# Kernel tuning notes

Measured on AMD Instinct MI355X. Metric: run time of the kernel, lower is better.

The kernel has to match this reference:

```python
import jax, jax.numpy as jnp
import numpy as np

EPS = 1e-6
NEG = 1e9

def _norm(x):
    # Normalizator math with alpha=1, gamma=0 (torch.std is unbiased -> ddof=1)
    m = jnp.mean(x, axis=-1, keepdims=True)
    s = jnp.std(x, axis=-1, ddof=1, keepdims=True)
    return (x - m) / (s + EPS)

def setup_inputs() -> dict:
    key = jax.random.key(0)
    ks = jax.random.split(key, 16)
    T, S, D, F, L = 4096, 4096, 512, 2048, 4
    sc = 1.0 / np.sqrt(D)
    scf = 1.0 / np.sqrt(F)
    return {
        "current_tgt_output": jax.random.normal(ks[0], (T, D), jnp.float32),
        "encoder_output": jax.random.normal(ks[1], (S, D), jnp.float32),
        "cross_mask": jax.random.randint(ks[2], (T, S), 0, 2).astype(jnp.float32),
        "Wq": jax.random.normal(ks[3], (L, D, D), jnp.float32) * sc,
        "Wk": jax.random.normal(ks[4], (L, D, D), jnp.float32) * sc,
        "Wv": jax.random.normal(ks[5], (L, D, D), jnp.float32) * sc,
        "Wo": jax.random.normal(ks[6], (L, D, D), jnp.float32) * sc,
        "Cq": jax.random.normal(ks[7], (L, D, D), jnp.float32) * sc,
        "Ck": jax.random.normal(ks[8], (L, D, D), jnp.float32) * sc,
        "Cv": jax.random.normal(ks[9], (L, D, D), jnp.float32) * sc,
        "Co": jax.random.normal(ks[10], (L, D, D), jnp.float32) * sc,
        "W1": jax.random.normal(ks[11], (L, D, F), jnp.float32) * sc,
        "W2": jax.random.normal(ks[12], (L, F, D), jnp.float32) * scf,
        "alpha": jnp.ones((1,), jnp.float32),
        "gamma": jnp.zeros((1,), jnp.float32),
        "input_ids": jax.random.randint(ks[13], (T,), 0, S),
        "training_step": T,
        "training_mode": 1,
    }

def reference(current_tgt_output, encoder_output, cross_mask, Wq, Wk, Wv, Wo,
              Cq, Ck, Cv, Co, W1, W2, alpha, gamma, input_ids,
              training_step, training_mode):
    T = training_step
    x = current_tgt_output[:T] if training_mode else current_tgt_output
    cm = cross_mask[:T]                                  # [T, S]
    # the python double-loop -> single vectorized gather: self_mask[i,k]=cross_mask[i, input_ids[k]]
    self_mask = cm[:, input_ids]                         # [T, T]
    sbias = (self_mask - 1.0) * NEG                      # additive mask bias
    cbias = (cm - 1.0) * NEG
    D = x.shape[-1]
    scale = 1.0 / jnp.sqrt(jnp.asarray(D, x.dtype))
    L = Wq.shape[0]
    for l in range(L):
        h = _norm(x)
        q, k, v = h @ Wq[l], h @ Wk[l], h @ Wv[l]
        a = jax.nn.softmax(q @ k.T * scale + sbias, axis=-1)
        x = x + (a @ v) @ Wo[l]
        h = _norm(x)
        q = h @ Cq[l]
        k, v = encoder_output @ Ck[l], encoder_output @ Cv[l]
        a = jax.nn.softmax(q @ k.T * scale + cbias, axis=-1)
        x = x + (a @ v) @ Co[l]
        h = _norm(x)
        x = x + jax.nn.relu(h @ W1[l]) @ W2[l]
    return alpha * _norm(x) + gamma
```

## Files before the change

kernel.cpp:

```cpp
#include <hip/hip_runtime.h>
#include <math.h>

typedef _Float16 half_t;
typedef unsigned int u32;
typedef unsigned short u16;
typedef float f32x4 __attribute__((ext_vector_type(4)));
typedef _Float16 f16x8 __attribute__((ext_vector_type(8)));
typedef _Float16 f16x4 __attribute__((ext_vector_type(4)));

#define T_DIM 4096
#define S_DIM 4096
#define D_DIM 512
#define F_DIM 2048
#define NLAYER 4
#define KVS ((size_t)4096 * 512)

__device__ __forceinline__ void gload16(const void* g, void* l) {
    __builtin_amdgcn_global_load_lds(
        (const __attribute__((address_space(1))) u32*)g,
        (__attribute__((address_space(3))) u32*)l, 16, 0, 0);
}

template<int N> __device__ __forceinline__ void wait_vm() {
    if constexpr (N == 0) asm volatile("s_waitcnt vmcnt(0)" ::: "memory");
    else if constexpr (N == 3) asm volatile("s_waitcnt vmcnt(3)" ::: "memory");
    else if constexpr (N == 4) asm volatile("s_waitcnt vmcnt(4)" ::: "memory");
    else if constexpr (N == 6) asm volatile("s_waitcnt vmcnt(6)" ::: "memory");
    else if constexpr (N == 8) asm volatile("s_waitcnt vmcnt(8)" ::: "memory");
}

template<int BN, int EPI>
__global__ __launch_bounds__(512)
void gemm_nt(const half_t* __restrict__ A, int lda,
             const half_t* __restrict__ B, int ldb,
             int N, int K, int gx,
             const float* __restrict__ Cin, float* __restrict__ Cout,
             half_t* __restrict__ D1, half_t* __restrict__ D2,
             half_t* __restrict__ D3, int ldd)
{
    constexpr int BM = 128, BK = 64;
    constexpr int NF = BN / 32;
    constexpr int LPT = 2 + BN / 64;
    constexpr int NSLOT = (BN == 64) ? 3 : 2;
    __shared__ half_t As[NSLOT][BM * BK];
    __shared__ half_t Bs[NSLOT][BN * BK];

    const int tid  = threadIdx.x;
    const int wave = tid >> 6;
    const int lane = tid & 63;

    const int nb  = gridDim.x;
    const int bid = blockIdx.x;
    const int nid = (bid & 7) * (nb >> 3) + (bid >> 3);
    const int gy  = nb / gx;
    const int bx  = nid % gx;
    const int by  = nid / gx % gy;
    const int bm = by * BM, bn = bx * BN;

    const int wm = (wave >> 1) * 32;
    const int wn = (wave & 1) * (BN / 2);
    const int kq = lane >> 4;
    const int rr = lane & 15;
    const int scol = (((lane & 7) ^ (lane >> 3)) << 3);

    f32x4 acc[2][NF];
#pragma unroll
    for (int m = 0; m < 2; ++m)
#pragma unroll
        for (int n = 0; n < NF; ++n)
            acc[m][n] = f32x4{0.f, 0.f, 0.f, 0.f};

    auto stage = [&](int buf, int k0) {
#pragma unroll
        for (int c = 0; c < 2; ++c) {
            const int row = wave * 16 + c * 8 + (lane >> 3);
            gload16(A + (size_t)(bm + row) * lda + k0 + scol,
                    (char*)&As[buf][0] + (wave * 2 + c) * 1024 + lane * 16);
        }
        if constexpr (BN == 64) {
            const int row = wave * 8 + (lane >> 3);
            gload16(B + (size_t)(bn + row) * ldb + k0 + scol,
                    (char*)&Bs[buf][0] + wave * 1024 + lane * 16);
        } else {
#pragma unroll
            for (int c = 0; c < 2; ++c) {
                const int row = wave * 16 + c * 8 + (lane >> 3);
                gload16(B + (size_t)(bn + row) * ldb + k0 + scol,
                        (char*)&Bs[buf][0] + (wave * 2 + c) * 1024 + lane * 16);
            }
        }
    };

    const int nt = K / BK;
    stage(0, 0);
    if constexpr (NSLOT == 3) stage(1, BK);
    int cur = 0, pf = NSLOT - 1;
    for (int t = 0; t < nt; ++t) {
        if (t + 1 < nt) wait_vm<(NSLOT - 2) * LPT>(); else wait_vm<0>();
        __builtin_amdgcn_s_barrier();
        if (t + NSLOT - 1 < nt) stage(pf, (t + NSLOT - 1) * BK);
#pragma unroll
        for (int ks = 0; ks < 2; ++ks) {
            f16x8 af[2], bf[NF];
#pragma unroll
            for (int m = 0; m < 2; ++m) {
                const int r = wm + m * 16 + rr;
                af[m] = *(const f16x8*)&As[cur][r * BK + (((ks * 4 + kq) ^ (r & 7)) << 3)];
            }
#pragma unroll
            for (int n = 0; n < NF; ++n) {
                const int r = wn + n * 16 + rr;
                bf[n] = *(const f16x8*)&Bs[cur][r * BK + (((ks * 4 + kq) ^ (r & 7)) << 3)];
            }
#pragma unroll
            for (int m = 0; m < 2; ++m)
#pragma unroll
                for (int n = 0; n < NF; ++n)
                    acc[m][n] = __builtin_amdgcn_mfma_f32_16x16x32_f16(af[m], bf[n], acc[m][n], 0, 0, 0);
        }
        cur = (cur + 1 == NSLOT) ? 0 : cur + 1;
        pf  = (pf  + 1 == NSLOT) ? 0 : pf  + 1;
    }

    const int r0 = bm + wm + (lane >> 4) * 4;
#pragma unroll
    for (int m = 0; m < 2; ++m)
#pragma unroll
        for (int n = 0; n < NF; ++n) {
            const int c = bn + wn + n * 16 + rr;
            if (EPI == 1) {
#pragma unroll
                for (int i = 0; i < 4; ++i) {
                    const int r = r0 + m * 16 + i;
                    Cout[(size_t)r * N + c] = Cin[(size_t)r * N + c] + acc[m][n][i];
                }
            } else if (EPI == 2) {
#pragma unroll
                for (int i = 0; i < 4; ++i)
                    D1[(size_t)(r0 + m * 16 + i) * ldd + c] = (half_t)acc[m][n][i];
            } else if (EPI == 5) {
                if (bn < 512) {
#pragma unroll
                    for (int i = 0; i < 4; ++i)
                        D1[(size_t)(r0 + m * 16 + i) * 512 + c] = (half_t)acc[m][n][i];
                } else if (bn < 1024) {
#pragma unroll
                    for (int i = 0; i < 4; ++i)
                        D2[(size_t)(r0 + m * 16 + i) * 512 + (c - 512)] = (half_t)acc[m][n][i];
                } else {
                    f16x4 hv;
#pragma unroll
                    for (int i = 0; i < 4; ++i) hv[i] = (half_t)acc[m][n][i];
                    *(f16x4*)&D3[(size_t)(c - 1024) * ldd + r0 + m * 16] = hv;
                }
            } else {
                const int l = c >> 10;
                const int sub = c & 1023;
                if (sub < 512) {
#pragma unroll
                    for (int i = 0; i < 4; ++i)
                        D2[l * KVS + (size_t)(r0 + m * 16 + i) * 512 + sub] = (half_t)acc[m][n][i];
                } else {
                    f16x4 hv;
#pragma unroll
                    for (int i = 0; i < 4; ++i) hv[i] = (half_t)acc[m][n][i];
                    *(f16x4*)&D3[l * KVS + (size_t)(sub - 512) * 4096 + r0 + m * 16] = hv;
                }
            }
        }
}

template<int EPI, int SPLITK = 1, int P16 = 1>
__global__ __launch_bounds__(256)
void gemm97(const half_t* __restrict__ A, int lda,
            const half_t* __restrict__ B, int ldb,
            int K, int gx, half_t* __restrict__ D,
            float* __restrict__ Fout, int ldd)
{
    constexpr int BK = 32, NSLOT = 3, LPT = 4;
    __shared__ half_t As[NSLOT][128 * BK];
    __shared__ half_t Bs[NSLOT][128 * BK];

    const int tid  = threadIdx.x;
    const int wave = tid >> 6;
    const int lane = tid & 63;

    const int nb  = gridDim.x;
    const int bid = blockIdx.x;
    const int nid = (bid & 7) * (nb >> 3) + (bid >> 3);
    const int gy  = nb / (gx * SPLITK);
    const int bx  = nid % gx;
    const int tmp = nid / gx;
    const int by  = tmp % gy;
    const int kz  = tmp / gy;
    const int bm = by * 128, bn = bx * 128;

    const int Keff = K / SPLITK;
    A += (size_t)kz * Keff;
    B += (size_t)kz * Keff;

    const int wm = (wave >> 1) * 64;
    const int wn = (wave & 1) * 64;
    const int kq = lane >> 4;
    const int rr = lane & 15;
    const int srow = lane >> 2;
    const int scol = (((lane & 3) ^ ((lane >> 3) & 3)) << 3);
    const int kqa  = kq ^ ((rr >> 1) & 3);

    const half_t* Abase = A + (size_t)(bm + wave * 16 + srow) * lda + scol;
    const half_t* Bbase = B + (size_t)(bn + wave * 16 + srow) * ldb + scol;

    f32x4 acc[4][4];
#pragma unroll
    for (int m = 0; m < 4; ++m)
#pragma unroll
        for (int n = 0; n < 4; ++n)
            acc[m][n] = f32x4{0.f, 0.f, 0.f, 0.f};

    auto stage = [&](int buf, int k0) {
#pragma unroll
        for (int c = 0; c < 2; ++c)
            gload16(Abase + (size_t)c * 64 * lda + k0,
                    (char*)&As[buf][0] + c * 4096 + wave * 1024 + lane * 16);
#pragma unroll
        for (int c = 0; c < 2; ++c)
            gload16(Bbase + (size_t)c * 64 * ldb + k0,
                    (char*)&Bs[buf][0] + c * 4096 + wave * 1024 + lane * 16);
    };

    const int nt = Keff / BK;
    stage(0, 0);
    stage(1, BK);
    int cur = 0, pf = 2;
    for (int t = 0; t < nt; ++t) {
        if (t + 1 < nt) wait_vm<LPT>(); else wait_vm<0>();
        __builtin_amdgcn_s_barrier();
        if (t + 2 < nt) stage(pf, (t + 2) * BK);
        f16x8 af[4], bf[4];
#pragma unroll
        for (int m = 0; m < 4; ++m)
            af[m] = *(const f16x8*)&As[cur][(wm + m * 16 + rr) * BK + kqa * 8];
#pragma unroll
        for (int n = 0; n < 4; ++n)
            bf[n] = *(const f16x8*)&Bs[cur][(wn + n * 16 + rr) * BK + kqa * 8];
#pragma unroll
        for (int m = 0; m < 4; ++m)
#pragma unroll
            for (int n = 0; n < 4; ++n)
                acc[m][n] = __builtin_amdgcn_mfma_f32_16x16x32_f16(af[m], bf[n], acc[m][n], 0, 0, 0);
        cur = (cur == 2) ? 0 : cur + 1;
        pf  = (pf  == 2) ? 0 : pf + 1;
    }

    const int r0 = bm + wm + (lane >> 4) * 4;
    const int soff = kz * gx * 128;
#pragma unroll
    for (int m = 0; m < 4; ++m)
#pragma unroll
        for (int n = 0; n < 4; ++n) {
            const int c = bn + wn + n * 16 + rr;
#pragma unroll
            for (int i = 0; i < 4; ++i) {
                float v = acc[m][n][i];
                const size_t r = r0 + m * 16 + i;
                if constexpr (SPLITK > 1) {
                    if constexpr (P16) D[r * ldd + soff + c] = (half_t)v;
                    else               Fout[r * ldd + soff + c] = v;
                } else {
                    if (EPI == 4) v = fmaxf(v, 0.f);
                    D[r * ldd + c] = (half_t)v;
                }
            }
        }
}

__global__ __launch_bounds__(256)
void reduce_p16(const half_t* __restrict__ P, half_t* __restrict__ ao)
{
    const size_t q = ((size_t)blockIdx.x * 256 + threadIdx.x) * 8;
    const size_t r = q >> 9;
    const int d = (int)(q & 511);
    const half_t* row = P + r * 2048 + d;
    float s[8] = {0.f};
#pragma unroll
    for (int j = 0; j < 4; ++j) {
        f16x8 v = *(const f16x8*)(row + j * 512);
#pragma unroll
        for (int e = 0; e < 8; ++e) s[e] += (float)v[e];
    }
    f16x8 o;
#pragma unroll
    for (int e = 0; e < 8; ++e) o[e] = (half_t)s[e];
    *(f16x8*)&ao[q] = o;
}

template<int FINAL>
__global__ __launch_bounds__(256)
void norm_red(const float* __restrict__ xin, const float* __restrict__ P,
              float* __restrict__ xbuf, half_t* __restrict__ hh,
              float* __restrict__ outF, const float* __restrict__ alphaP,
              const float* __restrict__ gammaP)
{
    const int row  = blockIdx.x * 4 + (threadIdx.x >> 6);
    const int lane = threadIdx.x & 63;
    const int d0 = lane * 8;
    const float* xr = xin + (size_t)row * D_DIM + d0;
    float v[8];
    {
        float4 a = *(const float4*)xr;
        float4 b = *(const float4*)(xr + 4);
        v[0]=a.x; v[1]=a.y; v[2]=a.z; v[3]=a.w; v[4]=b.x; v[5]=b.y; v[6]=b.z; v[7]=b.w;
    }
    const float* pr = P + (size_t)row * 2048 + d0;
#pragma unroll
    for (int j = 0; j < 4; ++j) {
        float4 a = *(const float4*)(pr + j * 512);
        float4 b = *(const float4*)(pr + j * 512 + 4);
        v[0]+=a.x; v[1]+=a.y; v[2]+=a.z; v[3]+=a.w; v[4]+=b.x; v[5]+=b.y; v[6]+=b.z; v[7]+=b.w;
    }
    float* xo = xbuf + (size_t)row * D_DIM + d0;
    *(float4*)xo       = float4{v[0], v[1], v[2], v[3]};
    *(float4*)(xo + 4) = float4{v[4], v[5], v[6], v[7]};

    float s = 0.f;
#pragma unroll
    for (int j = 0; j < 8; ++j) s += v[j];
#pragma unroll
    for (int off = 32; off; off >>= 1) s += __shfl_xor(s, off);
    const float mean = s * (1.f / 512.f);
    float ss = 0.f;
#pragma unroll
    for (int j = 0; j < 8; ++j) { float d = v[j] - mean; ss += d * d; }
#pragma unroll
    for (int off = 32; off; off >>= 1) ss += __shfl_xor(ss, off);
    const float inv = 1.f / (sqrtf(ss * (1.f / 511.f)) + 1e-6f);
    if (FINAL) {
        const float alp = alphaP[0], gam = gammaP[0];
        float o[8];
#pragma unroll
        for (int j = 0; j < 8; ++j) o[j] = alp * ((v[j] - mean) * inv) + gam;
        float* op = outF + (size_t)row * D_DIM + d0;
        *(float4*)op       = float4{o[0], o[1], o[2], o[3]};
        *(float4*)(op + 4) = float4{o[4], o[5], o[6], o[7]};
    } else {
        f16x8 hv;
#pragma unroll
        for (int j = 0; j < 8; ++j) hv[j] = (half_t)((v[j] - mean) * inv);
        *(f16x8*)&hh[(size_t)row * D_DIM + d0] = hv;
    }
}

template<int FINAL>
__global__ __launch_bounds__(256)
void norm_rows(const float* __restrict__ x, half_t* __restrict__ hh,
               float* __restrict__ outF, const float* __restrict__ alphaP,
               const float* __restrict__ gammaP)
{
    const int row  = blockIdx.x * 4 + (threadIdx.x >> 6);
    const int lane = threadIdx.x & 63;
    const float* xr = x + (size_t)row * D_DIM + lane * 8;
    float4 a = *(const float4*)xr;
    float4 b = *(const float4*)(xr + 4);
    float v[8] = {a.x, a.y, a.z, a.w, b.x, b.y, b.z, b.w};
    float s = 0.f;
#pragma unroll
    for (int j = 0; j < 8; ++j) s += v[j];
#pragma unroll
    for (int off = 32; off; off >>= 1) s += __shfl_xor(s, off);
    const float mean = s * (1.f / 512.f);
    float ss = 0.f;
#pragma unroll
    for (int j = 0; j < 8; ++j) { float d = v[j] - mean; ss += d * d; }
#pragma unroll
    for (int off = 32; off; off >>= 1) ss += __shfl_xor(ss, off);
    const float inv = 1.f / (sqrtf(ss * (1.f / 511.f)) + 1e-6f);
    if (FINAL) {
        const float alp = alphaP[0], gam = gammaP[0];
        float o[8];
#pragma unroll
        for (int j = 0; j < 8; ++j) o[j] = alp * ((v[j] - mean) * inv) + gam;
        float* op = outF + (size_t)row * D_DIM + lane * 8;
        *(float4*)op       = float4{o[0], o[1], o[2], o[3]};
        *(float4*)(op + 4) = float4{o[4], o[5], o[6], o[7]};
    } else {
        f16x8 hv;
#pragma unroll
        for (int j = 0; j < 8; ++j) hv[j] = (half_t)((v[j] - mean) * inv);
        *(f16x8*)&hh[(size_t)row * D_DIM + lane * 8] = hv;
    }
}

__global__ __launch_bounds__(256)
void cast_f16(const float* __restrict__ in, half_t* __restrict__ out)
{
    size_t i = ((size_t)blockIdx.x * 256 + threadIdx.x) * 8;
    float4 a = *(const float4*)&in[i];
    float4 b = *(const float4*)&in[i + 4];
    float v[8] = {a.x, a.y, a.z, a.w, b.x, b.y, b.z, b.w};
    f16x8 o;
#pragma unroll
    for (int j = 0; j < 8; ++j) o[j] = (half_t)v[j];
    *(f16x8*)&out[i] = o;
}

__global__ __launch_bounds__(256)
void transpose_cast(const float* __restrict__ in, half_t* __restrict__ out,
                    int R, int C, float scale, int inZ, int outZ)
{
    in  += (size_t)blockIdx.z * inZ;
    out += (size_t)blockIdx.z * outZ;
    __shared__ float tile[32][33];
    const int tx = threadIdx.x & 31, ty = threadIdx.x >> 5;
    const int r0 = blockIdx.y * 32, c0 = blockIdx.x * 32;
#pragma unroll
    for (int i = 0; i < 4; ++i)
        tile[ty + i * 8][tx] = in[(size_t)(r0 + ty + i * 8) * C + c0 + tx];
    __syncthreads();
#pragma unroll
    for (int i = 0; i < 4; ++i)
        out[(size_t)(c0 + ty + i * 8) * R + r0 + tx] = (half_t)(tile[tx][ty + i * 8] * scale);
}

__global__ __launch_bounds__(256)
void pack_masks(const float* __restrict__ cm, const int* __restrict__ ids,
                u32* __restrict__ crossb, u32* __restrict__ selfb)
{
    const int t = blockIdx.x;
    const float* row = cm + (size_t)t * S_DIM;
    __shared__ u32 cb[S_DIM / 32];
    __shared__ u16 sh16[256];
    const int tid = threadIdx.x;
    u32 bits = 0;
#pragma unroll
    for (int q = 0; q < 4; ++q) {
        float4 v = *(const float4*)&row[tid * 16 + q * 4];
        bits |= (v.x > 0.5f ? 1u : 0u) << (q * 4 + 0);
        bits |= (v.y > 0.5f ? 1u : 0u) << (q * 4 + 1);
        bits |= (v.z > 0.5f ? 1u : 0u) << (q * 4 + 2);
        bits |= (v.w > 0.5f ? 1u : 0u) << (q * 4 + 3);
    }
    ((u16*)cb)[tid] = (u16)bits;
    __syncthreads();
    u32 sb = 0;
#pragma unroll
    for (int q = 0; q < 4; ++q) {
        int4 id4 = *(const int4*)&ids[tid * 16 + q * 4];
        sb |= ((cb[id4.x >> 5] >> (id4.x & 31)) & 1u) << (q * 4 + 0);
        sb |= ((cb[id4.y >> 5] >> (id4.y & 31)) & 1u) << (q * 4 + 1);
        sb |= ((cb[id4.z >> 5] >> (id4.z & 31)) & 1u) << (q * 4 + 2);
        sb |= ((cb[id4.w >> 5] >> (id4.w & 31)) & 1u) << (q * 4 + 3);
    }
    sh16[tid] = (u16)sb;
    __syncthreads();
    if (tid < 128) {
        crossb[(size_t)t * 128 + tid] = cb[tid];
        selfb[(size_t)t * 128 + tid]  = (u32)sh16[2 * tid] | ((u32)sh16[2 * tid + 1] << 16);
    }
}

__global__ __launch_bounds__(256)
void softmax_rows16(half_t* __restrict__ logits, const u32* __restrict__ bits)
{
    const int t = blockIdx.x;
    half_t* row = logits + (size_t)t * S_DIM;
    const u32* bw = bits + (size_t)t * (S_DIM / 32);
    __shared__ float red[8];
    const int tid = threadIdx.x, wave = tid >> 6, lane = tid & 63;
    const int s0 = tid * 16;
    f16x8 h0 = *(const f16x8*)&row[s0];
    f16x8 h1 = *(const f16x8*)&row[s0 + 8];
    const u32 w = bw[tid >> 1] >> ((tid & 1) * 16);
    float z[16];
    float lmax = -3.0e38f;
#pragma unroll
    for (int q = 0; q < 16; ++q) {
        const float v = (float)((q < 8) ? h0[q & 7] : h1[q & 7]);
        z[q] = v + (((w >> q) & 1u) ? 0.f : -1e9f);
        lmax = fmaxf(lmax, z[q]);
    }
#pragma unroll
    for (int off = 32; off; off >>= 1) lmax = fmaxf(lmax, __shfl_xor(lmax, off));
    if (lane == 0) red[wave] = lmax;
    __syncthreads();
    const float mx = fmaxf(fmaxf(red[0], red[1]), fmaxf(red[2], red[3]));
    float lsum = 0.f;
#pragma unroll
    for (int q = 0; q < 16; ++q) { z[q] = __expf(z[q] - mx); lsum += z[q]; }
#pragma unroll
    for (int off = 32; off; off >>= 1) lsum += __shfl_xor(lsum, off);
    if (lane == 0) red[4 + wave] = lsum;
    __syncthreads();
    const float inv = 1.f / (red[4] + red[5] + red[6] + red[7]);
    f16x8 o0, o1;
#pragma unroll
    for (int q = 0; q < 8; ++q) {
        o0[q] = (half_t)(z[q] * inv);
        o1[q] = (half_t)(z[q + 8] * inv);
    }
    *(f16x8*)&row[s0] = o0;
    *(f16x8*)&row[s0 + 8] = o1;
}

extern "C" void kernel_launch(void* const* d_in, const int* in_sizes, int n_in,
                              void* d_out, int out_size, void* d_ws, size_t ws_size,
                              hipStream_t stream)
{
    (void)in_sizes; (void)n_in; (void)out_size; (void)ws_size;

    const float* x0p  = (const float*)d_in[0];
    const float* encp = (const float*)d_in[1];
    const float* cmp  = (const float*)d_in[2];
    const float* Wq = (const float*)d_in[3], *Wk = (const float*)d_in[4];
    const float* Wv = (const float*)d_in[5], *Wo = (const float*)d_in[6];
    const float* Cq = (const float*)d_in[7], *Ck = (const float*)d_in[8];
    const float* Cv = (const float*)d_in[9], *Co = (const float*)d_in[10];
    const float* W1p = (const float*)d_in[11];
    const float* W2p = (const float*)d_in[12];
    const float* alphap = (const float*)d_in[13];
    const float* gammap = (const float*)d_in[14];
    const int*   idsp   = (const int*)d_in[15];
    float* outp = (float*)d_out;

    char* wp = (char*)d_ws;
    auto take = [&](size_t nelem, int esz) -> void* {
        void* p = (void*)wp;
        wp += (nelem * (size_t)esz + 255) & ~(size_t)255;
        return p;
    };
    half_t* wqkvT = (half_t*)take((size_t)NLAYER * 1536 * 512, 2);
    half_t* ckvT  = (half_t*)take((size_t)NLAYER * 1024 * 512, 2);
    half_t* cqT   = (half_t*)take((size_t)NLAYER * 512 * 512, 2);
    half_t* woT   = (half_t*)take((size_t)NLAYER * 512 * 512, 2);
    half_t* coT   = (half_t*)take((size_t)NLAYER * 512 * 512, 2);
    half_t* w1T   = (half_t*)take((size_t)NLAYER * D_DIM * F_DIM, 2);
    half_t* w2T   = (half_t*)take((size_t)NLAYER * D_DIM * F_DIM, 2);
    half_t* hh    = (half_t*)take((size_t)T_DIM * D_DIM, 2);
    half_t* qb    = (half_t*)take((size_t)T_DIM * D_DIM, 2);
    half_t* kb    = (half_t*)take((size_t)S_DIM * D_DIM, 2);
    half_t* vT    = (half_t*)take((size_t)S_DIM * D_DIM, 2);
    half_t* ao    = (half_t*)take((size_t)T_DIM * D_DIM, 2);
    half_t* mid   = (half_t*)take((size_t)T_DIM * F_DIM, 2);
    half_t* enc16 = (half_t*)take((size_t)S_DIM * D_DIM, 2);
    half_t* kbC   = (half_t*)take((size_t)NLAYER * S_DIM * D_DIM, 2);
    half_t* vTC   = (half_t*)take((size_t)NLAYER * S_DIM * D_DIM, 2);
    float* xbuf   = (float*)take((size_t)T_DIM * D_DIM, 4);
    half_t* logit16 = (half_t*)take((size_t)T_DIM * S_DIM, 2);
    half_t* p16   = (half_t*)take((size_t)T_DIM * 2048, 2);
    float* pbuf   = (float*)take((size_t)T_DIM * 2048, 4);
    u32* crossb = (u32*)take((size_t)T_DIM * (S_DIM / 32), 4);
    u32* selfb  = (u32*)take((size_t)T_DIM * (S_DIM / 32), 4);

    const dim3 B(256), B512(512);
    const float qscale = 0.04419417382415922f;

    const int SQ = 512 * 512, QKVZ = 1536 * 512, KVZ = 1024 * 512, FZ = 512 * 2048;
    transpose_cast<<<dim3(16,16,4), B, 0, stream>>>(Wq, wqkvT,            512, 512, qscale, SQ, QKVZ);
    transpose_cast<<<dim3(16,16,4), B, 0, stream>>>(Wk, wqkvT + SQ,       512, 512, 1.f,    SQ, QKVZ);
    transpose_cast<<<dim3(16,16,4), B, 0, stream>>>(Wv, wqkvT + 2 * SQ,   512, 512, 1.f,    SQ, QKVZ);
    transpose_cast<<<dim3(16,16,4), B, 0, stream>>>(Wo, woT,              512, 512, 1.f,    SQ, SQ);
    transpose_cast<<<dim3(16,16,4), B, 0, stream>>>(Cq, cqT,              512, 512, qscale, SQ, SQ);
    transpose_cast<<<dim3(16,16,4), B, 0, stream>>>(Ck, ckvT,             512, 512, 1.f,    SQ, KVZ);
    transpose_cast<<<dim3(16,16,4), B, 0, stream>>>(Cv, ckvT + SQ,        512, 512, 1.f,    SQ, KVZ);
    transpose_cast<<<dim3(16,16,4), B, 0, stream>>>(Co, coT,              512, 512, 1.f,    SQ, SQ);
    transpose_cast<<<dim3(64,16,4), B, 0, stream>>>(W1p, w1T, 512, 2048, 1.f, FZ, FZ);
    transpose_cast<<<dim3(16,64,4), B, 0, stream>>>(W2p, w2T, 2048, 512, 1.f, FZ, FZ);
    cast_f16<<<dim3((S_DIM * D_DIM / 8) / 256), B, 0, stream>>>(encp, enc16);
    pack_masks<<<dim3(T_DIM), B, 0, stream>>>(cmp, idsp, crossb, selfb);
    gemm_nt<64, 7><<<dim3(2048), B512, 0, stream>>>(enc16, 512, ckvT, 512,
        4096, 512, 64, nullptr, nullptr, nullptr, kbC, vTC, 4096);

    for (int l = 0; l < NLAYER; ++l) {
        const float* xin = (l == 0) ? x0p : xbuf;

        if (l == 0)
            norm_rows<0><<<T_DIM / 4, B, 0, stream>>>(x0p, hh, nullptr, nullptr, nullptr);
        else
            norm_red<0><<<T_DIM / 4, B, 0, stream>>>(xbuf, pbuf, xbuf, hh, nullptr, nullptr, nullptr);

        gemm_nt<64, 5><<<dim3(768), B512, 0, stream>>>(hh, 512, wqkvT + (size_t)l * QKVZ, 512,
            1536, 512, 24, nullptr, nullptr, qb, kb, vT, 4096);
        gemm97<2><<<dim3(1024), B, 0, stream>>>(qb, 512, kb, 512, 512, 32, logit16, nullptr, 4096);
        softmax_rows16<<<dim3(T_DIM), B, 0, stream>>>(logit16, selfb);
        gemm97<0, 4, 1><<<dim3(512), B, 0, stream>>>(logit16, 4096, vT, 4096,
            4096, 4, p16, nullptr, 2048);
        reduce_p16<<<dim3(1024), B, 0, stream>>>(p16, ao);
        gemm_nt<64, 1><<<dim3(256), B512, 0, stream>>>(ao, 512, woT + (size_t)l * SQ, 512,
            512, 512, 8, xin, xbuf, nullptr, nullptr, nullptr, 0);

        norm_rows<0><<<T_DIM / 4, B, 0, stream>>>(xbuf, hh, nullptr, nullptr, nullptr);
        gemm_nt<64, 2><<<dim3(256), B512, 0, stream>>>(hh, 512, cqT + (size_t)l * SQ, 512,
            512, 512, 8, nullptr, nullptr, qb, nullptr, nullptr, 512);
        gemm97<2><<<dim3(1024), B, 0, stream>>>(qb, 512, kbC + (size_t)l * KVS, 512,
            512, 32, logit16, nullptr, 4096);
        softmax_rows16<<<dim3(T_DIM), B, 0, stream>>>(logit16, crossb);
        gemm97<0, 4, 1><<<dim3(512), B, 0, stream>>>(logit16, 4096, vTC + (size_t)l * KVS, 4096,
            4096, 4, p16, nullptr, 2048);
        reduce_p16<<<dim3(1024), B, 0, stream>>>(p16, ao);
        gemm_nt<64, 1><<<dim3(256), B512, 0, stream>>>(ao, 512, coT + (size_t)l * SQ, 512,
            512, 512, 8, xbuf, xbuf, nullptr, nullptr, nullptr, 0);

        norm_rows<0><<<T_DIM / 4, B, 0, stream>>>(xbuf, hh, nullptr, nullptr, nullptr);
        gemm97<4><<<dim3(512), B, 0, stream>>>(hh, 512, w1T + (size_t)l * FZ, 512,
            512, 16, mid, nullptr, 2048);
        gemm97<0, 4, 0><<<dim3(512), B, 0, stream>>>(mid, 2048, w2T + (size_t)l * FZ, 2048,
            2048, 4, nullptr, pbuf, 2048);
    }

    norm_red<1><<<T_DIM / 4, B, 0, stream>>>(xbuf, pbuf, xbuf, nullptr, outp, alphap, gammap);
}
```

Before: 1.091 ms.

## Fold output projections into V and fuse residual-add with layer norm

Uses (A·V)·Wo = A·(V·Wo) to precompute V·Wo, and Cv-projected encoder values times Co, with a new gemm_fold kernel that writes transposed values. This removes the per-attention reduce kernel and the output-projection GEMM. The split-K partial sums are now reduced in a fused attn_tail kernel that adds the residual and computes the next layer norm in one pass, replacing reduce_p16, the output projection and norm_rows. In exchange the V·Wo products are rounded to fp16 before the attention GEMM, which may change numerics slightly.

```diff
diff --git a/kernel.cpp b/kernel.cpp
--- a/kernel.cpp
+++ b/kernel.cpp
@@ -34,7 +34,6 @@
 void gemm_nt(const half_t* __restrict__ A, int lda,
              const half_t* __restrict__ B, int ldb,
              int N, int K, int gx,
-             const float* __restrict__ Cin, float* __restrict__ Cout,
              half_t* __restrict__ D1, half_t* __restrict__ D2,
              half_t* __restrict__ D3, int ldd)
 {
@@ -52,9 +51,8 @@
     const int nb  = gridDim.x;
     const int bid = blockIdx.x;
     const int nid = (bid & 7) * (nb >> 3) + (bid >> 3);
-    const int gy  = nb / gx;
     const int bx  = nid % gx;
-    const int by  = nid / gx % gy;
+    const int by  = nid / gx;
     const int bm = by * BM, bn = bx * BN;
 
     const int wm = (wave >> 1) * 32;
@@ -128,45 +126,115 @@
 #pragma unroll
         for (int n = 0; n < NF; ++n) {
             const int c = bn + wn + n * 16 + rr;
-            if (EPI == 1) {
-#pragma unroll
-                for (int i = 0; i < 4; ++i) {
-                    const int r = r0 + m * 16 + i;
-                    Cout[(size_t)r * N + c] = Cin[(size_t)r * N + c] + acc[m][n][i];
-                }
-            } else if (EPI == 2) {
+            if (EPI == 2) {
 #pragma unroll
                 for (int i = 0; i < 4; ++i)
                     D1[(size_t)(r0 + m * 16 + i) * ldd + c] = (half_t)acc[m][n][i];
             } else if (EPI == 5) {
-                if (bn < 512) {
-#pragma unroll
-                    for (int i = 0; i < 4; ++i)
-                        D1[(size_t)(r0 + m * 16 + i) * 512 + c] = (half_t)acc[m][n][i];
-                } else if (bn < 1024) {
-#pragma unroll
-                    for (int i = 0; i < 4; ++i)
-                        D2[(size_t)(r0 + m * 16 + i) * 512 + (c - 512)] = (half_t)acc[m][n][i];
-                } else {
-                    f16x4 hv;
-#pragma unroll
-                    for (int i = 0; i < 4; ++i) hv[i] = (half_t)acc[m][n][i];
-                    *(f16x4*)&D3[(size_t)(c - 1024) * ldd + r0 + m * 16] = hv;
-                }
+                half_t* Dst = (bn < 512) ? D1 : (bn < 1024) ? D2 : D3;
+                const int sub = c & 511;
+#pragma unroll
+                for (int i = 0; i < 4; ++i)
+                    Dst[(size_t)(r0 + m * 16 + i) * 512 + sub] = (half_t)acc[m][n][i];
             } else {
                 const int l = c >> 10;
                 const int sub = c & 1023;
-                if (sub < 512) {
-#pragma unroll
-                    for (int i = 0; i < 4; ++i)
-                        D2[l * KVS + (size_t)(r0 + m * 16 + i) * 512 + sub] = (half_t)acc[m][n][i];
-                } else {
-                    f16x4 hv;
-#pragma unroll
-                    for (int i = 0; i < 4; ++i) hv[i] = (half_t)acc[m][n][i];
-                    *(f16x4*)&D3[l * KVS + (size_t)(sub - 512) * 4096 + r0 + m * 16] = hv;
-                }
+                half_t* Dst = (sub < 512) ? (D2 + l * KVS) : (D3 + l * KVS);
+                const int d = sub & 511;
+#pragma unroll
+                for (int i = 0; i < 4; ++i)
+                    Dst[(size_t)(r0 + m * 16 + i) * 512 + d] = (half_t)acc[m][n][i];
             }
+        }
+}
+
+__global__ __launch_bounds__(512)
+void gemm_fold(const half_t* __restrict__ Wt, const half_t* __restrict__ V,
+               half_t* __restrict__ Out, int zSA, long zSB, long zSD)
+{
+    constexpr int BM = 128, BK = 64, BN = 64, NSLOT = 3, LPT = 3;
+    __shared__ half_t As[NSLOT][BM * BK];
+    __shared__ half_t Bs[NSLOT][BN * BK];
+
+    const half_t* A = Wt + (size_t)blockIdx.z * zSA;
+    const half_t* B = V  + (size_t)blockIdx.z * zSB;
+    half_t* D = Out + (size_t)blockIdx.z * zSD;
+
+    const int tid  = threadIdx.x;
+    const int wave = tid >> 6;
+    const int lane = tid & 63;
+
+    const int nb  = gridDim.x;
+    const int bid = blockIdx.x;
+    const int nid = (bid & 7) * (nb >> 3) + (bid >> 3);
+    const int bx = nid & 63, by = nid >> 6;
+    const int bm = by * BM, bn = bx * BN;
+
+    const int wm = (wave >> 1) * 32;
+    const int wn = (wave & 1) * 32;
+    const int kq = lane >> 4;
+    const int rr = lane & 15;
+    const int scol = (((lane & 7) ^ (lane >> 3)) << 3);
+
+    f32x4 acc[2][2];
+#pragma unroll
+    for (int m = 0; m < 2; ++m)
+#pragma unroll
+        for (int n = 0; n < 2; ++n)
+            acc[m][n] = f32x4{0.f, 0.f, 0.f, 0.f};
+
+    auto stage = [&](int buf, int k0) {
+#pragma unroll
+        for (int c = 0; c < 2; ++c) {
+            const int row = wave * 16 + c * 8 + (lane >> 3);
+            gload16(A + (size_t)(bm + row) * 512 + k0 + scol,
+                    (char*)&As[buf][0] + (wave * 2 + c) * 1024 + lane * 16);
+        }
+        const int row = wave * 8 + (lane >> 3);
+        gload16(B + (size_t)(bn + row) * 512 + k0 + scol,
+                (char*)&Bs[buf][0] + wave * 1024 + lane * 16);
+    };
+
+    const int nt = 512 / BK;
+    stage(0, 0);
+    stage(1, BK);
+    int cur = 0, pf = 2;
+    for (int t = 0; t < nt; ++t) {
+        if (t + 1 < nt) wait_vm<LPT>(); else wait_vm<0>();
+        __builtin_amdgcn_s_barrier();
+        if (t + 2 < nt) stage(pf, (t + 2) * BK);
+#pragma unroll
+        for (int ks = 0; ks < 2; ++ks) {
+            f16x8 af[2], bf[2];
+#pragma unroll
+            for (int m = 0; m < 2; ++m) {
+                const int r = wm + m * 16 + rr;
+                af[m] = *(const f16x8*)&As[cur][r * BK + (((ks * 4 + kq) ^ (r & 7)) << 3)];
+            }
+#pragma unroll
+            for (int n = 0; n < 2; ++n) {
+                const int r = wn + n * 16 + rr;
+                bf[n] = *(const f16x8*)&Bs[cur][r * BK + (((ks * 4 + kq) ^ (r & 7)) << 3)];
+            }
+#pragma unroll
+            for (int m = 0; m < 2; ++m)
+#pragma unroll
+                for (int n = 0; n < 2; ++n)
+                    acc[m][n] = __builtin_amdgcn_mfma_f32_16x16x32_f16(af[m], bf[n], acc[m][n], 0, 0, 0);
+        }
+        cur = (cur + 1 == NSLOT) ? 0 : cur + 1;
+        pf  = (pf  + 1 == NSLOT) ? 0 : pf  + 1;
+    }
+
+    const int r0 = bm + wm + (lane >> 4) * 4;
+#pragma unroll
+    for (int m = 0; m < 2; ++m)
+#pragma unroll
+        for (int n = 0; n < 2; ++n) {
+            const int c = bn + wn + n * 16 + rr;
+#pragma unroll
+            for (int i = 0; i < 4; ++i)
+                D[(size_t)(r0 + m * 16 + i) * 4096 + c] = (half_t)acc[m][n][i];
         }
 }
 
@@ -275,23 +343,46 @@
 }
 
 __global__ __launch_bounds__(256)
-void reduce_p16(const half_t* __restrict__ P, half_t* __restrict__ ao)
-{
-    const size_t q = ((size_t)blockIdx.x * 256 + threadIdx.x) * 8;
-    const size_t r = q >> 9;
-    const int d = (int)(q & 511);
-    const half_t* row = P + r * 2048 + d;
-    float s[8] = {0.f};
+void attn_tail(const float* __restrict__ xin, const half_t* __restrict__ P,
+               float* __restrict__ xbuf, half_t* __restrict__ hh)
+{
+    const int row  = blockIdx.x * 4 + (threadIdx.x >> 6);
+    const int lane = threadIdx.x & 63;
+    const int d0 = lane * 8;
+    float v[8];
+    {
+        const float* xr = xin + (size_t)row * D_DIM + d0;
+        float4 a = *(const float4*)xr;
+        float4 b = *(const float4*)(xr + 4);
+        v[0]=a.x; v[1]=a.y; v[2]=a.z; v[3]=a.w; v[4]=b.x; v[5]=b.y; v[6]=b.z; v[7]=b.w;
+    }
+    const half_t* pr = P + (size_t)row * 2048 + d0;
 #pragma unroll
     for (int j = 0; j < 4; ++j) {
-        f16x8 v = *(const f16x8*)(row + j * 512);
-#pragma unroll
-        for (int e = 0; e < 8; ++e) s[e] += (float)v[e];
-    }
-    f16x8 o;
-#pragma unroll
-    for (int e = 0; e < 8; ++e) o[e] = (half_t)s[e];
-    *(f16x8*)&ao[q] = o;
+        f16x8 pv = *(const f16x8*)(pr + j * 512);
+#pragma unroll
+        for (int e = 0; e < 8; ++e) v[e] += (float)pv[e];
+    }
+    float* xo = xbuf + (size_t)row * D_DIM + d0;
+    *(float4*)xo       = float4{v[0], v[1], v[2], v[3]};
+    *(float4*)(xo + 4) = float4{v[4], v[5], v[6], v[7]};
+
+    float s = 0.f;
+#pragma unroll
+    for (int j = 0; j < 8; ++j) s += v[j];
+#pragma unroll
+    for (int off = 32; off; off >>= 1) s += __shfl_xor(s, off);
+    const float mean = s * (1.f / 512.f);
+    float ss = 0.f;
+#pragma unroll
+    for (int j = 0; j < 8; ++j) { float d = v[j] - mean; ss += d * d; }
+#pragma unroll
+    for (int off = 32; off; off >>= 1) ss += __shfl_xor(ss, off);
+    const float inv = 1.f / (sqrtf(ss * (1.f / 511.f)) + 1e-6f);
+    f16x8 hv;
+#pragma unroll
+    for (int j = 0; j < 8; ++j) hv[j] = (half_t)((v[j] - mean) * inv);
+    *(f16x8*)&hh[(size_t)row * D_DIM + d0] = hv;
 }
 
 template<int FINAL>
@@ -318,10 +409,11 @@
         float4 b = *(const float4*)(pr + j * 512 + 4);
         v[0]+=a.x; v[1]+=a.y; v[2]+=a.z; v[3]+=a.w; v[4]+=b.x; v[5]+=b.y; v[6]+=b.z; v[7]+=b.w;
     }
-    float* xo = xbuf + (size_t)row * D_DIM + d0;
-    *(float4*)xo       = float4{v[0], v[1], v[2], v[3]};
-    *(float4*)(xo + 4) = float4{v[4], v[5], v[6], v[7]};
-
+    if (!FINAL) {
+        float* xo = xbuf + (size_t)row * D_DIM + d0;
+        *(float4*)xo       = float4{v[0], v[1], v[2], v[3]};
+        *(float4*)(xo + 4) = float4{v[4], v[5], v[6], v[7]};
+    }
     float s = 0.f;
 #pragma unroll
     for (int j = 0; j < 8; ++j) s += v[j];
@@ -537,12 +629,13 @@
     half_t* hh    = (half_t*)take((size_t)T_DIM * D_DIM, 2);
     half_t* qb    = (half_t*)take((size_t)T_DIM * D_DIM, 2);
     half_t* kb    = (half_t*)take((size_t)S_DIM * D_DIM, 2);
-    half_t* vT    = (half_t*)take((size_t)S_DIM * D_DIM, 2);
-    half_t* ao    = (half_t*)take((size_t)T_DIM * D_DIM, 2);
+    half_t* vb    = (half_t*)take((size_t)S_DIM * D_DIM, 2);
+    half_t* vTp   = (half_t*)take((size_t)S_DIM * D_DIM, 2);
     half_t* mid   = (half_t*)take((size_t)T_DIM * F_DIM, 2);
     half_t* enc16 = (half_t*)take((size_t)S_DIM * D_DIM, 2);
     half_t* kbC   = (half_t*)take((size_t)NLAYER * S_DIM * D_DIM, 2);
-    half_t* vTC   = (half_t*)take((size_t)NLAYER * S_DIM * D_DIM, 2);
+    half_t* vC    = (half_t*)take((size_t)NLAYER * S_DIM * D_DIM, 2);
+    half_t* vTCp  = (half_t*)take((size_t)NLAYER * S_DIM * D_DIM, 2);
     float* xbuf   = (float*)take((size_t)T_DIM * D_DIM, 4);
     half_t* logit16 = (half_t*)take((size_t)T_DIM * S_DIM, 2);
     half_t* p16   = (half_t*)take((size_t)T_DIM * 2048, 2);
@@ -567,39 +660,34 @@
     cast_f16<<<dim3((S_DIM * D_DIM / 8) / 256), B, 0, stream>>>(encp, enc16);
     pack_masks<<<dim3(T_DIM), B, 0, stream>>>(cmp, idsp, crossb, selfb);
     gemm_nt<64, 7><<<dim3(2048), B512, 0, stream>>>(enc16, 512, ckvT, 512,
-        4096, 512, 64, nullptr, nullptr, nullptr, kbC, vTC, 4096);
+        4096, 512, 64, nullptr, kbC, vC, 0);
+    gemm_fold<<<dim3(256, 1, NLAYER), B512, 0, stream>>>(coT, vC, vTCp,
+        SQ, (long)KVS, (long)KVS);
 
     for (int l = 0; l < NLAYER; ++l) {
-        const float* xin = (l == 0) ? x0p : xbuf;
-
         if (l == 0)
             norm_rows<0><<<T_DIM / 4, B, 0, stream>>>(x0p, hh, nullptr, nullptr, nullptr);
         else
             norm_red<0><<<T_DIM / 4, B, 0, stream>>>(xbuf, pbuf, xbuf, hh, nullptr, nullptr, nullptr);
 
         gemm_nt<64, 5><<<dim3(768), B512, 0, stream>>>(hh, 512, wqkvT + (size_t)l * QKVZ, 512,
-            1536, 512, 24, nullptr, nullptr, qb, kb, vT, 4096);
+            1536, 512, 24, qb, kb, vb, 0);
+        gemm_fold<<<dim3(256, 1, 1), B512, 0, stream>>>(woT + (size_t)l * SQ, vb, vTp, 0, 0, 0);
         gemm97<2><<<dim3(1024), B, 0, stream>>>(qb, 512, kb, 512, 512, 32, logit16, nullptr, 4096);
         softmax_rows16<<<dim3(T_DIM), B, 0, stream>>>(logit16, selfb);
-        gemm97<0, 4, 1><<<dim3(512), B, 0, stream>>>(logit16, 4096, vT, 4096,
+        gemm97<0, 4, 1><<<dim3(512), B, 0, stream>>>(logit16, 4096, vTp, 4096,
             4096, 4, p16, nullptr, 2048);
-        reduce_p16<<<dim3(1024), B, 0, stream>>>(p16, ao);
-        gemm_nt<64, 1><<<dim3(256), B512, 0, stream>>>(ao, 512, woT + (size_t)l * SQ, 512,
-            512, 512, 8, xin, xbuf, nullptr, nullptr, nullptr, 0);
-
-        norm_rows<0><<<T_DIM / 4, B, 0, stream>>>(xbuf, hh, nullptr, nullptr, nullptr);
+        attn_tail<<<dim3(T_DIM / 4), B, 0, stream>>>((l == 0) ? x0p : xbuf, p16, xbuf, hh);
+
         gemm_nt<64, 2><<<dim3(256), B512, 0, stream>>>(hh, 512, cqT + (size_t)l * SQ, 512,
-            512, 512, 8, nullptr, nullptr, qb, nullptr, nullptr, 512);
+            512, 512, 8, qb, nullptr, nullptr, 512);
         gemm97<2><<<dim3(1024), B, 0, stream>>>(qb, 512, kbC + (size_t)l * KVS, 512,
             512, 32, logit16, nullptr, 4096);
         softmax_rows16<<<dim3(T_DIM), B, 0, stream>>>(logit16, crossb);
-        gemm97<0, 4, 1><<<dim3(512), B, 0, stream>>>(logit16, 4096, vTC + (size_t)l * KVS, 4096,
+        gemm97<0, 4, 1><<<dim3(512), B, 0, stream>>>(logit16, 4096, vTCp + (size_t)l * KVS, 4096,
             4096, 4, p16, nullptr, 2048);
-        reduce_p16<<<dim3(1024), B, 0, stream>>>(p16, ao);
-        gemm_nt<64, 1><<<dim3(256), B512, 0, stream>>>(ao, 512, coT + (size_t)l * SQ, 512,
-            512, 512, 8, xbuf, xbuf, nullptr, nullptr, nullptr, 0);
-
-        norm_rows<0><<<T_DIM / 4, B, 0, stream>>>(xbuf, hh, nullptr, nullptr, nullptr);
+        attn_tail<<<dim3(T_DIM / 4), B, 0, stream>>>(xbuf, p16, xbuf, hh);
+
         gemm97<4><<<dim3(512), B, 0, stream>>>(hh, 512, w1T + (size_t)l * FZ, 512,
             512, 16, mid, nullptr, 2048);
         gemm97<0, 4, 0><<<dim3(512), B, 0, stream>>>(mid, 2048, w2T + (size_t)l * FZ, 2048,
```

Result: no change. 1.100 ms (+0.9%).
